# Performance work log

Hardware: AMD Instinct MI355X
Metric: run time of the kernel (lower is better)

Reference implementation:

```python
import jax, jax.numpy as jnp
import numpy as np

B, S, H = 64, 512, 768
NUM_BD = 5
N_CLASSES = 9
N_REGIONS = 4096
GAMMA = 0.3


def setup_inputs() -> dict:
    key = jax.random.key(0)
    ks = jax.random.split(key, 11)
    return {
        "word_repr": jax.random.normal(ks[0], (B, S, H), dtype=jnp.float32),
        "W_s": jax.random.normal(ks[1], (H, NUM_BD), dtype=jnp.float32) * 0.02,
        "b_s": jax.random.normal(ks[2], (NUM_BD,), dtype=jnp.float32) * 0.02,
        "W_r": jax.random.normal(ks[3], (H, N_CLASSES), dtype=jnp.float32) * 0.02,
        "b_r": jax.random.normal(ks[4], (N_CLASSES,), dtype=jnp.float32) * 0.02,
        "bd_tgt": jax.random.randint(ks[5], (B, S), 0, NUM_BD),
        "seg": jax.random.randint(ks[6], (B, S), 0, 2),
        "region_starts": jax.random.randint(ks[7], (N_REGIONS,), 0, 495),
        "region_lengths": jax.random.randint(ks[8], (N_REGIONS,), 0, 16),
        "region_batch": jax.random.randint(ks[9], (N_REGIONS,), 0, B),
        "region_labels": jax.random.randint(ks[10], (N_REGIONS,), 0, N_CLASSES),
    }


def reference(word_repr, W_s, b_s, W_r, b_r, bd_tgt, seg,
              region_starts, region_lengths, region_batch, region_labels):
    dt = word_repr.dtype
    b, s, h = word_repr.shape

    # sentence boundary logits [B,S,5]
    sent_out = jnp.einsum('bsh,hk->bsk', word_repr, W_s) + b_s

    # --- region mean pooling via exclusive prefix sums (fused segment-mean) ---
    cs = jnp.concatenate(
        [jnp.zeros((b, 1, h), dt), jnp.cumsum(word_repr, axis=1)], axis=1)  # [B,S+1,H]
    ends = region_starts + region_lengths  # inclusive end index
    seg_sum = cs[region_batch, ends + 1] - cs[region_batch, region_starts]  # [R,H]
    lens = (region_lengths + 1).astype(dt)
    region_repr = seg_sum / lens[:, None]

    # region classification + cross-entropy (mean)
    region_logits = region_repr @ W_r + b_r  # [R,C]
    logp_r = jax.nn.log_softmax(region_logits, axis=-1)
    ent_loss = -jnp.mean(
        jnp.take_along_axis(logp_r, region_labels[:, None], axis=1)[:, 0])

    # boundary loss: masked mean NLL with one-hot targets
    logp_s = jax.nn.log_softmax(sent_out.reshape(-1, NUM_BD), axis=-1)
    nll = -jnp.take_along_axis(logp_s, bd_tgt.reshape(-1, 1), axis=1)[:, 0]
    mask = seg.reshape(-1).astype(dt)
    bd_loss = jnp.sum(mask * nll) / (jnp.sum(mask) + 1e-6)

    return GAMMA * ent_loss + (1.0 - GAMMA) * bd_loss
```

## Files before the change

### kernel.cpp

```cpp
#include <hip/hip_runtime.h>

#define BB 64
#define SS 512
#define HH 768
#define NBD 5
#define NC 9
#define NR 4096

__global__ __launch_bounds__(256) void bd_kernel(
    const float* __restrict__ wr, const float* __restrict__ Ws,
    const float* __restrict__ bs, const int* __restrict__ tgt,
    const int* __restrict__ seg, float2* __restrict__ out_part)
{
    const int wid  = threadIdx.x >> 6;
    const int lane = threadIdx.x & 63;
    const int gw   = blockIdx.x * 4 + wid;

    float wreg[3][4][NBD];
    #pragma unroll
    for (int j = 0; j < 3; ++j)
        #pragma unroll
        for (int e = 0; e < 4; ++e) {
            const int h = 4 * lane + 256 * j + e;
            #pragma unroll
            for (int k = 0; k < NBD; ++k)
                wreg[j][e][k] = Ws[h * NBD + k];
        }

    float b0 = bs[0], b1 = bs[1], b2 = bs[2], b3 = bs[3], b4 = bs[4];

    float nll_sum = 0.f, msk_sum = 0.f;

    #pragma unroll
    for (int i = 0; i < 4; ++i) {
        const int token = gw + 8192 * i;
        const float4* row4 = (const float4*)(wr + (size_t)token * HH);

        float4 v[3];
        #pragma unroll
        for (int j = 0; j < 3; ++j) v[j] = row4[lane + 64 * j];

        float dot[NBD] = {0.f, 0.f, 0.f, 0.f, 0.f};
        #pragma unroll
        for (int j = 0; j < 3; ++j) {
            const float x[4] = {v[j].x, v[j].y, v[j].z, v[j].w};
            #pragma unroll
            for (int e = 0; e < 4; ++e)
                #pragma unroll
                for (int k = 0; k < NBD; ++k)
                    dot[k] += x[e] * wreg[j][e][k];
        }

        #pragma unroll
        for (int k = 0; k < NBD; ++k)
            #pragma unroll
            for (int off = 32; off; off >>= 1)
                dot[k] += __shfl_xor(dot[k], off);

        if (lane == 0) {
            float l[NBD] = {dot[0] + b0, dot[1] + b1, dot[2] + b2,
                            dot[3] + b3, dot[4] + b4};
            float m = l[0];
            #pragma unroll
            for (int k = 1; k < NBD; ++k) m = fmaxf(m, l[k]);
            float ssum = 0.f;
            #pragma unroll
            for (int k = 0; k < NBD; ++k) ssum += expf(l[k] - m);
            const float lse = logf(ssum);
            const int   t   = tgt[token];
            const float msk = (float)seg[token];
            nll_sum += msk * (-(l[t] - m - lse));
            msk_sum += msk;
        }
    }

    __shared__ float s_n[4], s_m[4];
    if (lane == 0) { s_n[wid] = nll_sum; s_m[wid] = msk_sum; }
    __syncthreads();
    if (threadIdx.x == 0) {
        out_part[blockIdx.x] =
            make_float2(s_n[0] + s_n[1] + s_n[2] + s_n[3],
                        s_m[0] + s_m[1] + s_m[2] + s_m[3]);
    }
}

__global__ __launch_bounds__(192) void region_kernel(
    const float* __restrict__ wr, const float* __restrict__ Wr,
    const float* __restrict__ br, const int* __restrict__ rstart,
    const int* __restrict__ rlen, const int* __restrict__ rbatch,
    const int* __restrict__ rlabel, float* __restrict__ out_nll)
{
    const int r    = blockIdx.x;
    const int tid  = threadIdx.x;
    const int wid  = tid >> 6;
    const int lane = tid & 63;

    const int start = rstart[r];
    const int len   = rlen[r] + 1;
    const int b     = rbatch[r];

    const float4* base4 =
        (const float4*)wr + ((size_t)b * SS + start) * (HH / 4);

    float s0 = 0.f, s1 = 0.f, s2 = 0.f, s3 = 0.f;
    for (int row = 0; row < len; ++row) {
        const float4 v = base4[row * (HH / 4) + tid];
        s0 += v.x; s1 += v.y; s2 += v.z; s3 += v.w;
    }
    const float inv = 1.0f / (float)len;
    const float m[4] = {s0 * inv, s1 * inv, s2 * inv, s3 * inv};

    float part[NC];
    #pragma unroll
    for (int c = 0; c < NC; ++c) part[c] = 0.f;
    #pragma unroll
    for (int e = 0; e < 4; ++e) {
        const int h = 4 * tid + e;
        #pragma unroll
        for (int c = 0; c < NC; ++c) part[c] += m[e] * Wr[h * NC + c];
    }

    #pragma unroll
    for (int c = 0; c < NC; ++c)
        #pragma unroll
        for (int off = 32; off; off >>= 1)
            part[c] += __shfl_xor(part[c], off);

    __shared__ float red[3][NC];
    if (lane == 0) {
        #pragma unroll
        for (int c = 0; c < NC; ++c) red[wid][c] = part[c];
    }
    __syncthreads();

    if (tid == 0) {
        float l[NC];
        #pragma unroll
        for (int c = 0; c < NC; ++c)
            l[c] = red[0][c] + red[1][c] + red[2][c] + br[c];
        float mx = l[0];
        #pragma unroll
        for (int c = 1; c < NC; ++c) mx = fmaxf(mx, l[c]);
        float ssum = 0.f;
        #pragma unroll
        for (int c = 0; c < NC; ++c) ssum += expf(l[c] - mx);
        const float lse = logf(ssum);
        const int   t   = rlabel[r];
        out_nll[r] = -(l[t] - mx - lse);
    }
}

__global__ __launch_bounds__(256) void fin_kernel(
    const float2* __restrict__ bdp, const float* __restrict__ rnll,
    float* __restrict__ out)
{
    const int tid  = threadIdx.x;
    const int wid  = tid >> 6;
    const int lane = tid & 63;

    double a = 0.0, c = 0.0, e = 0.0;
    for (int i = tid; i < 2048; i += 256) {
        const float2 p = bdp[i];
        a += (double)p.x;
        c += (double)p.y;
    }
    for (int i = tid; i < 4096; i += 256) e += (double)rnll[i];

    #pragma unroll
    for (int off = 32; off; off >>= 1) {
        a += __shfl_xor(a, off);
        c += __shfl_xor(c, off);
        e += __shfl_xor(e, off);
    }

    __shared__ double sa[4], sc[4], se[4];
    if (lane == 0) { sa[wid] = a; sc[wid] = c; se[wid] = e; }
    __syncthreads();

    if (tid == 0) {
        const double A = sa[0] + sa[1] + sa[2] + sa[3];
        const double C = sc[0] + sc[1] + sc[2] + sc[3];
        const double E = se[0] + se[1] + se[2] + se[3];
        const float ent = (float)(E / (double)NR);
        const float bd  = (float)(A / (C + 1e-6));
        out[0] = 0.3f * ent + 0.7f * bd;
    }
}

extern "C" void kernel_launch(void* const* d_in, const int* in_sizes, int n_in,
                              void* d_out, int out_size, void* d_ws, size_t ws_size,
                              hipStream_t stream)
{
    const float* wr     = (const float*)d_in[0];
    const float* Ws     = (const float*)d_in[1];
    const float* bs     = (const float*)d_in[2];
    const float* Wr     = (const float*)d_in[3];
    const float* br     = (const float*)d_in[4];
    const int*   tgt    = (const int*)d_in[5];
    const int*   seg    = (const int*)d_in[6];
    const int*   rstart = (const int*)d_in[7];
    const int*   rlen   = (const int*)d_in[8];
    const int*   rbatch = (const int*)d_in[9];
    const int*   rlabel = (const int*)d_in[10];

    float2* bdp  = (float2*)d_ws;
    float*  rnll = (float*)((char*)d_ws + 2048 * sizeof(float2));

    bd_kernel<<<2048, 256, 0, stream>>>(wr, Ws, bs, tgt, seg, bdp);
    region_kernel<<<NR, 192, 0, stream>>>(wr, Wr, br, rstart, rlen, rbatch,
                                          rlabel, rnll);
    fin_kernel<<<1, 256, 0, stream>>>(bdp, rnll, (float*)d_out);
}
```

Measured before the change: 190.3 us.

## Fuse boundary and region kernels into one interleaved launch with row-parallel pooling

Merges the boundary-loss and region-pooling kernels into a single launch. One third of the blocks do the boundary work and the rest do regions, interleaved so both run concurrently and share L2 reuse of word_repr. Region pooling now spreads rows across 4 waves, each reading a full row with float4, then reduces through shared memory. Weight loads are vectorised as float4. This removes a launch and the serialization between the two kernels, but adds divergent block roles and larger shared memory per block.

```diff
diff --git a/kernel.cpp b/kernel.cpp
--- a/kernel.cpp
+++ b/kernel.cpp
@@ -6,147 +6,180 @@
 #define NBD 5
 #define NC 9
 #define NR 4096
-
-__global__ __launch_bounds__(256) void bd_kernel(
+#define NB_BD 2048
+#define NBLK (NB_BD + NR)
+
+__global__ __launch_bounds__(256) void main_kernel(
     const float* __restrict__ wr, const float* __restrict__ Ws,
     const float* __restrict__ bs, const int* __restrict__ tgt,
-    const int* __restrict__ seg, float2* __restrict__ out_part)
+    const int* __restrict__ seg,
+    const float* __restrict__ Wr, const float* __restrict__ br,
+    const int* __restrict__ rstart, const int* __restrict__ rlen,
+    const int* __restrict__ rbatch, const int* __restrict__ rlabel,
+    float2* __restrict__ bd_part, float* __restrict__ rnll)
 {
-    const int wid  = threadIdx.x >> 6;
-    const int lane = threadIdx.x & 63;
-    const int gw   = blockIdx.x * 4 + wid;
-
-    float wreg[3][4][NBD];
-    #pragma unroll
-    for (int j = 0; j < 3; ++j)
-        #pragma unroll
-        for (int e = 0; e < 4; ++e) {
-            const int h = 4 * lane + 256 * j + e;
-            #pragma unroll
-            for (int k = 0; k < NBD; ++k)
-                wreg[j][e][k] = Ws[h * NBD + k];
-        }
-
-    float b0 = bs[0], b1 = bs[1], b2 = bs[2], b3 = bs[3], b4 = bs[4];
-
-    float nll_sum = 0.f, msk_sum = 0.f;
-
-    #pragma unroll
-    for (int i = 0; i < 4; ++i) {
-        const int token = gw + 8192 * i;
-        const float4* row4 = (const float4*)(wr + (size_t)token * HH);
-
-        float4 v[3];
-        #pragma unroll
-        for (int j = 0; j < 3; ++j) v[j] = row4[lane + 64 * j];
-
-        float dot[NBD] = {0.f, 0.f, 0.f, 0.f, 0.f};
-        #pragma unroll
-        for (int j = 0; j < 3; ++j) {
-            const float x[4] = {v[j].x, v[j].y, v[j].z, v[j].w};
-            #pragma unroll
-            for (int e = 0; e < 4; ++e)
-                #pragma unroll
-                for (int k = 0; k < NBD; ++k)
-                    dot[k] += x[e] * wreg[j][e][k];
-        }
-
-        #pragma unroll
-        for (int k = 0; k < NBD; ++k)
-            #pragma unroll
-            for (int off = 32; off; off >>= 1)
-                dot[k] += __shfl_xor(dot[k], off);
-
-        if (lane == 0) {
-            float l[NBD] = {dot[0] + b0, dot[1] + b1, dot[2] + b2,
-                            dot[3] + b3, dot[4] + b4};
-            float m = l[0];
-            #pragma unroll
-            for (int k = 1; k < NBD; ++k) m = fmaxf(m, l[k]);
-            float ssum = 0.f;
-            #pragma unroll
-            for (int k = 0; k < NBD; ++k) ssum += expf(l[k] - m);
-            const float lse = logf(ssum);
-            const int   t   = tgt[token];
-            const float msk = (float)seg[token];
-            nll_sum += msk * (-(l[t] - m - lse));
-            msk_sum += msk;
-        }
-    }
-
-    __shared__ float s_n[4], s_m[4];
-    if (lane == 0) { s_n[wid] = nll_sum; s_m[wid] = msk_sum; }
-    __syncthreads();
-    if (threadIdx.x == 0) {
-        out_part[blockIdx.x] =
-            make_float2(s_n[0] + s_n[1] + s_n[2] + s_n[3],
-                        s_m[0] + s_m[1] + s_m[2] + s_m[3]);
-    }
-}
-
-__global__ __launch_bounds__(192) void region_kernel(
-    const float* __restrict__ wr, const float* __restrict__ Wr,
-    const float* __restrict__ br, const int* __restrict__ rstart,
-    const int* __restrict__ rlen, const int* __restrict__ rbatch,
-    const int* __restrict__ rlabel, float* __restrict__ out_nll)
-{
-    const int r    = blockIdx.x;
     const int tid  = threadIdx.x;
     const int wid  = tid >> 6;
     const int lane = tid & 63;
-
-    const int start = rstart[r];
-    const int len   = rlen[r] + 1;
-    const int b     = rbatch[r];
-
-    const float4* base4 =
-        (const float4*)wr + ((size_t)b * SS + start) * (HH / 4);
-
-    float s0 = 0.f, s1 = 0.f, s2 = 0.f, s3 = 0.f;
-    for (int row = 0; row < len; ++row) {
-        const float4 v = base4[row * (HH / 4) + tid];
-        s0 += v.x; s1 += v.y; s2 += v.z; s3 += v.w;
-    }
-    const float inv = 1.0f / (float)len;
-    const float m[4] = {s0 * inv, s1 * inv, s2 * inv, s3 * inv};
-
-    float part[NC];
-    #pragma unroll
-    for (int c = 0; c < NC; ++c) part[c] = 0.f;
-    #pragma unroll
-    for (int e = 0; e < 4; ++e) {
-        const int h = 4 * tid + e;
+    const int bid  = blockIdx.x;
+
+    if (bid % 3 == 0) {
+        const int bb = bid / 3;
+        const int gw = bb * 4 + wid;
+
+        float wreg[3][4][NBD];
         #pragma unroll
-        for (int c = 0; c < NC; ++c) part[c] += m[e] * Wr[h * NC + c];
-    }
-
-    #pragma unroll
-    for (int c = 0; c < NC; ++c)
+        for (int j = 0; j < 3; ++j) {
+            const float4* wp = (const float4*)(Ws + (4 * lane + 256 * j) * NBD);
+            #pragma unroll
+            for (int p = 0; p < 5; ++p) {
+                const float4 f = wp[p];
+                const float vv[4] = {f.x, f.y, f.z, f.w};
+                #pragma unroll
+                for (int q = 0; q < 4; ++q) {
+                    const int flat = 4 * p + q;
+                    wreg[j][flat / NBD][flat % NBD] = vv[q];
+                }
+            }
+        }
+
+        const float b0 = bs[0], b1 = bs[1], b2 = bs[2], b3 = bs[3], b4 = bs[4];
+
+        float nll_sum = 0.f, msk_sum = 0.f;
+
         #pragma unroll
-        for (int off = 32; off; off >>= 1)
-            part[c] += __shfl_xor(part[c], off);
-
-    __shared__ float red[3][NC];
-    if (lane == 0) {
-        #pragma unroll
-        for (int c = 0; c < NC; ++c) red[wid][c] = part[c];
-    }
-    __syncthreads();
-
-    if (tid == 0) {
-        float l[NC];
-        #pragma unroll
-        for (int c = 0; c < NC; ++c)
-            l[c] = red[0][c] + red[1][c] + red[2][c] + br[c];
-        float mx = l[0];
-        #pragma unroll
-        for (int c = 1; c < NC; ++c) mx = fmaxf(mx, l[c]);
-        float ssum = 0.f;
-        #pragma unroll
-        for (int c = 0; c < NC; ++c) ssum += expf(l[c] - mx);
-        const float lse = logf(ssum);
-        const int   t   = rlabel[r];
-        out_nll[r] = -(l[t] - mx - lse);
+        for (int i = 0; i < 4; ++i) {
+            const int token = gw + 8192 * i;
+            const float4* row4 = (const float4*)(wr + (size_t)token * HH);
+
+            float4 v[3];
+            #pragma unroll
+            for (int j = 0; j < 3; ++j) v[j] = row4[lane + 64 * j];
+
+            float dot[NBD] = {0.f, 0.f, 0.f, 0.f, 0.f};
+            #pragma unroll
+            for (int j = 0; j < 3; ++j) {
+                const float x[4] = {v[j].x, v[j].y, v[j].z, v[j].w};
+                #pragma unroll
+                for (int e = 0; e < 4; ++e)
+                    #pragma unroll
+                    for (int k = 0; k < NBD; ++k)
+                        dot[k] += x[e] * wreg[j][e][k];
+            }
+
+            #pragma unroll
+            for (int k = 0; k < NBD; ++k)
+                #pragma unroll
+                for (int off = 32; off; off >>= 1)
+                    dot[k] += __shfl_xor(dot[k], off);
+
+            if (lane == 0) {
+                float l[NBD] = {dot[0] + b0, dot[1] + b1, dot[2] + b2,
+                                dot[3] + b3, dot[4] + b4};
+                float m = l[0];
+                #pragma unroll
+                for (int k = 1; k < NBD; ++k) m = fmaxf(m, l[k]);
+                float ssum = 0.f;
+                #pragma unroll
+                for (int k = 0; k < NBD; ++k) ssum += expf(l[k] - m);
+                const float lse = logf(ssum);
+                const int   t   = tgt[token];
+                const float msk = (float)seg[token];
+                nll_sum += msk * (-(l[t] - m - lse));
+                msk_sum += msk;
+            }
+        }
+
+        __shared__ float s_n[4], s_m[4];
+        if (lane == 0) { s_n[wid] = nll_sum; s_m[wid] = msk_sum; }
+        __syncthreads();
+        if (tid == 0) {
+            bd_part[bb] = make_float2(s_n[0] + s_n[1] + s_n[2] + s_n[3],
+                                      s_m[0] + s_m[1] + s_m[2] + s_m[3]);
+        }
+    } else {
+        const int r     = bid - bid / 3 - 1;
+        const int start = rstart[r];
+        const int len   = rlen[r] + 1;
+        const int b     = rbatch[r];
+
+        const float4* base4 =
+            (const float4*)wr + ((size_t)b * SS + start) * (HH / 4);
+
+        float4 a0 = {0.f, 0.f, 0.f, 0.f};
+        float4 a1 = {0.f, 0.f, 0.f, 0.f};
+        float4 a2 = {0.f, 0.f, 0.f, 0.f};
+        for (int row = wid; row < len; row += 4) {
+            const float4* p = base4 + (size_t)row * (HH / 4);
+            const float4 u0 = p[lane];
+            const float4 u1 = p[lane + 64];
+            const float4 u2 = p[lane + 128];
+            a0.x += u0.x; a0.y += u0.y; a0.z += u0.z; a0.w += u0.w;
+            a1.x += u1.x; a1.y += u1.y; a1.z += u1.z; a1.w += u1.w;
+            a2.x += u2.x; a2.y += u2.y; a2.z += u2.z; a2.w += u2.w;
+        }
+
+        __shared__ float4 partsh[4][192];
+        partsh[wid][lane]       = a0;
+        partsh[wid][lane + 64]  = a1;
+        partsh[wid][lane + 128] = a2;
+        __syncthreads();
+
+        __shared__ float redc[3][NC];
+        if (tid < 192) {
+            const float4 s0 = partsh[0][tid];
+            const float4 s1 = partsh[1][tid];
+            const float4 s2 = partsh[2][tid];
+            const float4 s3 = partsh[3][tid];
+            const float inv = 1.0f / (float)len;
+            const float m[4] = {(s0.x + s1.x + s2.x + s3.x) * inv,
+                                (s0.y + s1.y + s2.y + s3.y) * inv,
+                                (s0.z + s1.z + s2.z + s3.z) * inv,
+                                (s0.w + s1.w + s2.w + s3.w) * inv};
+
+            const float4* wrt = (const float4*)(Wr + 36 * tid);
+            float part[NC];
+            #pragma unroll
+            for (int c = 0; c < NC; ++c) part[c] = 0.f;
+            #pragma unroll
+            for (int j = 0; j < 9; ++j) {
+                const float4 f = wrt[j];
+                const float vv[4] = {f.x, f.y, f.z, f.w};
+                #pragma unroll
+                for (int q = 0; q < 4; ++q) {
+                    const int flat = 4 * j + q;
+                    part[flat % NC] += m[flat / NC] * vv[q];
+                }
+            }
+
+            #pragma unroll
+            for (int c = 0; c < NC; ++c)
+                #pragma unroll
+                for (int off = 32; off; off >>= 1)
+                    part[c] += __shfl_xor(part[c], off);
+
+            if (lane == 0) {
+                #pragma unroll
+                for (int c = 0; c < NC; ++c) redc[wid][c] = part[c];
+            }
+        }
+        __syncthreads();
+
+        if (tid == 0) {
+            float l[NC];
+            #pragma unroll
+            for (int c = 0; c < NC; ++c)
+                l[c] = redc[0][c] + redc[1][c] + redc[2][c] + br[c];
+            float mx = l[0];
+            #pragma unroll
+            for (int c = 1; c < NC; ++c) mx = fmaxf(mx, l[c]);
+            float ssum = 0.f;
+            #pragma unroll
+            for (int c = 0; c < NC; ++c) ssum += expf(l[c] - mx);
+            const float lse = logf(ssum);
+            const int   t   = rlabel[r];
+            rnll[r] = -(l[t] - mx - lse);
+        }
     }
 }
 
@@ -159,12 +192,12 @@
     const int lane = tid & 63;
 
     double a = 0.0, c = 0.0, e = 0.0;
-    for (int i = tid; i < 2048; i += 256) {
+    for (int i = tid; i < NB_BD; i += 256) {
         const float2 p = bdp[i];
         a += (double)p.x;
         c += (double)p.y;
     }
-    for (int i = tid; i < 4096; i += 256) e += (double)rnll[i];
+    for (int i = tid; i < NR; i += 256) e += (double)rnll[i];
 
     #pragma unroll
     for (int off = 32; off; off >>= 1) {
@@ -204,10 +237,10 @@
     const int*   rlabel = (const int*)d_in[10];
 
     float2* bdp  = (float2*)d_ws;
-    float*  rnll = (float*)((char*)d_ws + 2048 * sizeof(float2));
-
-    bd_kernel<<<2048, 256, 0, stream>>>(wr, Ws, bs, tgt, seg, bdp);
-    region_kernel<<<NR, 192, 0, stream>>>(wr, Wr, br, rstart, rlen, rbatch,
-                                          rlabel, rnll);
+    float*  rnll = (float*)((char*)d_ws + NB_BD * sizeof(float2));
+
+    main_kernel<<<NBLK, 256, 0, stream>>>(wr, Ws, bs, tgt, seg,
+                                          Wr, br, rstart, rlen, rbatch, rlabel,
+                                          bdp, rnll);
     fin_kernel<<<1, 256, 0, stream>>>(bdp, rnll, (float*)d_out);
 }
```

New measurement: 190.3 us. Within noise of the previous version (-0.0%).

## Batch row loads in boundary kernel, one wave per region, reorder launches

Applied to the files above, without the earlier changes.

The boundary kernel now issues all four token-row loads up front, on four consecutive tokens per wave instead of tokens strided by 8192, and loads the weights as float4. The region kernel assigns one wave per region, fully unrolls a 16-row loop with clamped loads and zero weights past the region length, and reads the classifier weights as float4, which removes the shared-memory reduction and block barrier. The region kernel is now launched before the boundary kernel. The aim is more memory-level parallelism and less synchronisation, at the cost of redundant row loads for short regions and higher register use.

```diff
diff --git a/kernel.cpp b/kernel.cpp
--- a/kernel.cpp
+++ b/kernel.cpp
@@ -3,9 +3,11 @@
 #define BB 64
 #define SS 512
 #define HH 768
+#define HH4 (HH / 4)
 #define NBD 5
 #define NC 9
 #define NR 4096
+#define NTOK (BB * SS)
 
 __global__ __launch_bounds__(256) void bd_kernel(
     const float* __restrict__ wr, const float* __restrict__ Ws,
@@ -18,32 +20,37 @@
 
     float wreg[3][4][NBD];
     #pragma unroll
-    for (int j = 0; j < 3; ++j)
-        #pragma unroll
-        for (int e = 0; e < 4; ++e) {
-            const int h = 4 * lane + 256 * j + e;
-            #pragma unroll
-            for (int k = 0; k < NBD; ++k)
-                wreg[j][e][k] = Ws[h * NBD + k];
-        }
-
-    float b0 = bs[0], b1 = bs[1], b2 = bs[2], b3 = bs[3], b4 = bs[4];
+    for (int j = 0; j < 3; ++j) {
+        const float4* wp = (const float4*)(Ws + (4 * lane + 256 * j) * NBD);
+        #pragma unroll
+        for (int p = 0; p < 5; ++p) {
+            const float4 f = wp[p];
+            const float vv[4] = {f.x, f.y, f.z, f.w};
+            #pragma unroll
+            for (int q = 0; q < 4; ++q) {
+                const int flat = 4 * p + q;
+                wreg[j][flat / NBD][flat % NBD] = vv[q];
+            }
+        }
+    }
+    const float b0 = bs[0], b1 = bs[1], b2 = bs[2], b3 = bs[3], b4 = bs[4];
+
+    const float4* base = (const float4*)wr + (size_t)(4 * gw) * HH4;
+    float4 v[4][3];
+    #pragma unroll
+    for (int i = 0; i < 4; ++i)
+        #pragma unroll
+        for (int j = 0; j < 3; ++j)
+            v[i][j] = base[i * HH4 + lane + 64 * j];
 
     float nll_sum = 0.f, msk_sum = 0.f;
 
     #pragma unroll
     for (int i = 0; i < 4; ++i) {
-        const int token = gw + 8192 * i;
-        const float4* row4 = (const float4*)(wr + (size_t)token * HH);
-
-        float4 v[3];
-        #pragma unroll
-        for (int j = 0; j < 3; ++j) v[j] = row4[lane + 64 * j];
-
         float dot[NBD] = {0.f, 0.f, 0.f, 0.f, 0.f};
         #pragma unroll
         for (int j = 0; j < 3; ++j) {
-            const float x[4] = {v[j].x, v[j].y, v[j].z, v[j].w};
+            const float x[4] = {v[i][j].x, v[i][j].y, v[i][j].z, v[i][j].w};
             #pragma unroll
             for (int e = 0; e < 4; ++e)
                 #pragma unroll
@@ -58,6 +65,7 @@
                 dot[k] += __shfl_xor(dot[k], off);
 
         if (lane == 0) {
+            const int token = 4 * gw + i;
             float l[NBD] = {dot[0] + b0, dot[1] + b1, dot[2] + b2,
                             dot[3] + b3, dot[4] + b4};
             float m = l[0];
@@ -84,40 +92,61 @@
     }
 }
 
-__global__ __launch_bounds__(192) void region_kernel(
+__global__ __launch_bounds__(256) void region_kernel(
     const float* __restrict__ wr, const float* __restrict__ Wr,
     const float* __restrict__ br, const int* __restrict__ rstart,
     const int* __restrict__ rlen, const int* __restrict__ rbatch,
     const int* __restrict__ rlabel, float* __restrict__ out_nll)
 {
-    const int r    = blockIdx.x;
-    const int tid  = threadIdx.x;
-    const int wid  = tid >> 6;
-    const int lane = tid & 63;
-
-    const int start = rstart[r];
-    const int len   = rlen[r] + 1;
-    const int b     = rbatch[r];
-
-    const float4* base4 =
-        (const float4*)wr + ((size_t)b * SS + start) * (HH / 4);
-
-    float s0 = 0.f, s1 = 0.f, s2 = 0.f, s3 = 0.f;
-    for (int row = 0; row < len; ++row) {
-        const float4 v = base4[row * (HH / 4) + tid];
-        s0 += v.x; s1 += v.y; s2 += v.z; s3 += v.w;
-    }
-    const float inv = 1.0f / (float)len;
-    const float m[4] = {s0 * inv, s1 * inv, s2 * inv, s3 * inv};
+    const int wid  = threadIdx.x >> 6;
+    const int lane = threadIdx.x & 63;
+    const int r    = blockIdx.x * 4 + wid;
+
+    const int   start = rstart[r];
+    const int   len   = rlen[r] + 1;
+    const int   b     = rbatch[r];
+    const float inv   = 1.0f / (float)len;
+
+    const float4* base =
+        (const float4*)wr + ((size_t)b * SS + start) * HH4;
+
+    float4 m0 = {0.f, 0.f, 0.f, 0.f};
+    float4 m1 = {0.f, 0.f, 0.f, 0.f};
+    float4 m2 = {0.f, 0.f, 0.f, 0.f};
+
+    #pragma unroll
+    for (int row = 0; row < 16; ++row) {
+        const int rc = (row < len) ? row : (len - 1);
+        const float4 u0 = base[(size_t)rc * HH4 + lane];
+        const float4 u1 = base[(size_t)rc * HH4 + lane + 64];
+        const float4 u2 = base[(size_t)rc * HH4 + lane + 128];
+        const float  w  = (row < len) ? inv : 0.f;
+        m0.x += w * u0.x; m0.y += w * u0.y; m0.z += w * u0.z; m0.w += w * u0.w;
+        m1.x += w * u1.x; m1.y += w * u1.y; m1.z += w * u1.z; m1.w += w * u1.w;
+        m2.x += w * u2.x; m2.y += w * u2.y; m2.z += w * u2.z; m2.w += w * u2.w;
+    }
 
     float part[NC];
     #pragma unroll
     for (int c = 0; c < NC; ++c) part[c] = 0.f;
-    #pragma unroll
-    for (int e = 0; e < 4; ++e) {
-        const int h = 4 * tid + e;
-        #pragma unroll
-        for (int c = 0; c < NC; ++c) part[c] += m[e] * Wr[h * NC + c];
+
+    const float mv[3][4] = {{m0.x, m0.y, m0.z, m0.w},
+                            {m1.x, m1.y, m1.z, m1.w},
+                            {m2.x, m2.y, m2.z, m2.w}};
+    #pragma unroll
+    for (int g = 0; g < 3; ++g) {
+        const int f = lane + 64 * g;
+        const float4* wv = (const float4*)(Wr + (size_t)4 * f * NC);
+        #pragma unroll
+        for (int j = 0; j < 9; ++j) {
+            const float4 x = wv[j];
+            const float vv[4] = {x.x, x.y, x.z, x.w};
+            #pragma unroll
+            for (int q = 0; q < 4; ++q) {
+                const int flat = 4 * j + q;
+                part[flat % NC] += mv[g][flat / NC] * vv[q];
+            }
+        }
     }
 
     #pragma unroll
@@ -126,18 +155,10 @@
         for (int off = 32; off; off >>= 1)
             part[c] += __shfl_xor(part[c], off);
 
-    __shared__ float red[3][NC];
     if (lane == 0) {
-        #pragma unroll
-        for (int c = 0; c < NC; ++c) red[wid][c] = part[c];
-    }
-    __syncthreads();
-
-    if (tid == 0) {
         float l[NC];
         #pragma unroll
-        for (int c = 0; c < NC; ++c)
-            l[c] = red[0][c] + red[1][c] + red[2][c] + br[c];
+        for (int c = 0; c < NC; ++c) l[c] = part[c] + br[c];
         float mx = l[0];
         #pragma unroll
         for (int c = 1; c < NC; ++c) mx = fmaxf(mx, l[c]);
@@ -164,7 +185,7 @@
         a += (double)p.x;
         c += (double)p.y;
     }
-    for (int i = tid; i < 4096; i += 256) e += (double)rnll[i];
+    for (int i = tid; i < NR; i += 256) e += (double)rnll[i];
 
     #pragma unroll
     for (int off = 32; off; off >>= 1) {
@@ -206,8 +227,8 @@
     float2* bdp  = (float2*)d_ws;
     float*  rnll = (float*)((char*)d_ws + 2048 * sizeof(float2));
 
-    bd_kernel<<<2048, 256, 0, stream>>>(wr, Ws, bs, tgt, seg, bdp);
-    region_kernel<<<NR, 192, 0, stream>>>(wr, Wr, br, rstart, rlen, rbatch,
-                                          rlabel, rnll);
+    region_kernel<<<NR / 4, 256, 0, stream>>>(wr, Wr, br, rstart, rlen,
+                                              rbatch, rlabel, rnll);
+    bd_kernel<<<NTOK / 16, 256, 0, stream>>>(wr, Ws, bs, tgt, seg, bdp);
     fin_kernel<<<1, 256, 0, stream>>>(bdp, rnll, (float*)d_out);
 }
```

Result: slower. 195.3 us (+2.7%).
